# Optimization experiments

Measured on AMD Instinct MI355X. Metric: run time of the kernel, lower is better.

## Reference

```python
import jax, jax.numpy as jnp
import numpy as np

N_HEADS = 4


def grid_sample_bilinear(img, grid):
    # img: (B, C, H, W); grid: (B, *S, 2) with (x, y) in [-1, 1]; torch bilinear, align_corners=True
    B, C, H, W = img.shape
    sp = grid.shape[1:-1]
    g = grid.reshape(B, -1, 2)
    x = (g[..., 0] + 1.0) * 0.5 * (W - 1)
    y = (g[..., 1] + 1.0) * 0.5 * (H - 1)
    x0 = jnp.floor(x)
    y0 = jnp.floor(y)
    wx = x - x0
    wy = y - y0
    x0i = jnp.clip(x0, 0, W - 1).astype(jnp.int32)
    x1i = jnp.clip(x0 + 1, 0, W - 1).astype(jnp.int32)
    y0i = jnp.clip(y0, 0, H - 1).astype(jnp.int32)
    y1i = jnp.clip(y0 + 1, 0, H - 1).astype(jnp.int32)
    flat = img.reshape(B, C, H * W)
    take = jax.vmap(lambda f, i: f[:, i])  # (C, HW), (N,) -> (C, N)
    out = (take(flat, y0i * W + x0i) * ((1 - wx) * (1 - wy))[:, None, :]
           + take(flat, y0i * W + x1i) * (wx * (1 - wy))[:, None, :]
           + take(flat, y1i * W + x0i) * ((1 - wx) * wy)[:, None, :]
           + take(flat, y1i * W + x1i) * (wx * wy)[:, None, :])
    return out.reshape((B, C) + sp)


def dw_conv_k4s4(x, w, b):
    # depthwise conv, kernel=4, stride=4, pad=0 (kernel == stride): non-overlapping patches
    B, C, H, W = x.shape
    xr = x.reshape(B, C, H // 4, 4, W // 4, 4)
    return jnp.einsum('bchpwq,cpq->bchw', xr, w) + b[None, :, None, None]


def ln_channels(x, g, b, eps=1e-5):
    # LayerNormProxy: LayerNorm over channel dim of NCHW
    mu = jnp.mean(x, axis=1, keepdims=True)
    var = jnp.var(x, axis=1, keepdims=True)
    return (x - mu) * jax.lax.rsqrt(var + eps) * g[None, :, None, None] + b[None, :, None, None]


def ref_points(Hk, Wk):
    ry = jnp.linspace(0.5, Hk - 0.5, Hk) / (Hk - 1.0) * 2.0 - 1.0
    rx = jnp.linspace(0.5, Wk - 0.5, Wk) / (Wk - 1.0) * 2.0 - 1.0
    return jnp.stack(jnp.meshgrid(ry, rx, indexing='ij'), axis=-1)  # (Hk, Wk, 2) as (y, x)


def q_grid(H, W):
    ry = jnp.arange(H, dtype=jnp.float32) / (H - 1.0) * 2.0 - 1.0
    rx = jnp.arange(W, dtype=jnp.float32) / (W - 1.0) * 2.0 - 1.0
    return jnp.stack(jnp.meshgrid(ry, rx, indexing='ij'), axis=-1).reshape(H * W, 2)


def dat_block(x, p):
    # DAttentionBaseline: n_groups=1, stride=ksize=4, offset_range_factor=-1, use_pe (learned rpe table)
    dw_w, dw_b, ln_g, ln_b, pw_w, wq, bq, wk, bk, wv, bv, wo, bo, rpe = p
    B, C, H, W = x.shape
    hc = C // N_HEADS
    scale = hc ** -0.5
    q = jnp.einsum('oc,bchw->bohw', wq, x) + bq[None, :, None, None]
    t = jax.nn.gelu(ln_channels(dw_conv_k4s4(q, dw_w, dw_b), ln_g, ln_b), approximate=False)
    off = jnp.einsum('oc,bchw->bohw', pw_w, t)  # (B, 2, Hk, Wk), channels = (dy, dx)
    Hk, Wk = off.shape[2], off.shape[3]
    ns = Hk * Wk
    pos = jnp.clip(off.transpose(0, 2, 3, 1) + ref_points(Hk, Wk)[None], -1.0, 1.0)  # (B,Hk,Wk,2) (y,x)
    xs = grid_sample_bilinear(x, pos[..., ::-1]).reshape(B, C, ns)  # kv == q input here
    k = jnp.einsum('oc,bcn->bon', wk, xs) + bk[None, :, None]
    v = jnp.einsum('oc,bcn->bon', wv, xs) + bv[None, :, None]
    qh = q.reshape(B, N_HEADS, hc, H * W)
    attn = jnp.einsum('bhcm,bhcn->bhmn', qh, k.reshape(B, N_HEADS, hc, ns)) * scale
    disp = (q_grid(H, W)[None, :, None, :] - pos.reshape(B, 1, ns, 2)) * 0.5  # (B, HW, ns, 2) (y,x)
    rpe_b = jnp.broadcast_to(rpe[None], (B,) + rpe.shape)
    attn = attn + grid_sample_bilinear(rpe_b, disp[..., ::-1])  # (B, heads, HW, ns)
    attn = jax.nn.softmax(attn, axis=-1)
    out = jnp.einsum('bhmn,bhcn->bhcm', attn, v.reshape(B, N_HEADS, hc, ns)).reshape(B, C, H, W)
    return jnp.einsum('oc,bchw->bohw', wo, out) + bo[None, :, None, None]


def _block_params(key, c, H, W):
    ks = jax.random.split(key, 7)
    return dict(
        off_dw_w=0.05 * jax.random.normal(ks[0], (c, 4, 4), dtype=jnp.float32),
        off_dw_b=jnp.zeros((c,), jnp.float32),
        ln_g=jnp.ones((c,), jnp.float32),
        ln_b=jnp.zeros((c,), jnp.float32),
        off_pw_w=0.02 * jax.random.normal(ks[1], (2, c), dtype=jnp.float32),
        wq=0.02 * jax.random.normal(ks[2], (c, c), dtype=jnp.float32),
        bq=jnp.zeros((c,), jnp.float32),
        wk=0.02 * jax.random.normal(ks[3], (c, c), dtype=jnp.float32),
        bk=jnp.zeros((c,), jnp.float32),
        wv=0.02 * jax.random.normal(ks[4], (c, c), dtype=jnp.float32),
        bv=jnp.zeros((c,), jnp.float32),
        wo=0.02 * jax.random.normal(ks[5], (c, c), dtype=jnp.float32),
        bo=jnp.zeros((c,), jnp.float32),
        rpe=0.01 * jax.random.normal(ks[6], (N_HEADS, 2 * H - 1, 2 * W - 1), dtype=jnp.float32),
    )


def setup_inputs() -> dict:
    key = jax.random.key(0)
    k0, k1, k2 = jax.random.split(key, 3)
    B, C, H, W = 8, 512, 64, 64
    inp = {'x0': jax.random.normal(k0, (B, C, H, W), dtype=jnp.float32)}
    for pre, k in (('sc_', k1), ('tr_', k2)):
        for n, v in _block_params(k, C // 2, H, W).items():
            inp[pre + n] = v
    return inp


def reference(x0,
              sc_off_dw_w, sc_off_dw_b, sc_ln_g, sc_ln_b, sc_off_pw_w, sc_wq, sc_bq, sc_wk, sc_bk,
              sc_wv, sc_bv, sc_wo, sc_bo, sc_rpe,
              tr_off_dw_w, tr_off_dw_b, tr_ln_g, tr_ln_b, tr_off_pw_w, tr_wq, tr_bq, tr_wk, tr_bk,
              tr_wv, tr_bv, tr_wo, tr_bo, tr_rpe):
    B, C, H, W = x0.shape
    qc1 = C // 2
    q = x0[:, :qc1]
    sc_p = (sc_off_dw_w, sc_off_dw_b, sc_ln_g, sc_ln_b, sc_off_pw_w, sc_wq, sc_bq, sc_wk, sc_bk,
            sc_wv, sc_bv, sc_wo, sc_bo, sc_rpe)
    tr_p = (tr_off_dw_w, tr_off_dw_b, tr_ln_g, tr_ln_b, tr_off_pw_w, tr_wq, tr_bq, tr_wk, tr_bk,
            tr_wv, tr_bv, tr_wo, tr_bo, tr_rpe)
    s = dat_block(q, sc_p)
    t = dat_block(q, tr_p)
    z = jnp.zeros((B, C - qc1, H, W), x0.dtype)
    scale_full = jnp.concatenate([z, s], axis=1)
    trans_full = jnp.concatenate([z, t], axis=1)
    res = x0 * jnp.exp(scale_full) + trans_full
    jac = jnp.sum(scale_full, axis=(1, 2, 3))[None, :]  # (n_vars=1, B)
    return res, jac
```

## Files before the change

### kernel.cpp

```cpp
#include <hip/hip_runtime.h>
#include <math.h>

typedef __bf16 bf16;
typedef __attribute__((ext_vector_type(8))) __bf16 bf16x8;
typedef __attribute__((ext_vector_type(4))) __bf16 bf16x4;
typedef __attribute__((ext_vector_type(4))) float floatx4;

#define MFMA16(a, b, c) __builtin_amdgcn_mfma_f32_16x16x32_bf16((a), (b), (c), 0, 0, 0)

__device__ __forceinline__ float bflo(unsigned d) {
    unsigned u = d << 16; float f; __builtin_memcpy(&f, &u, 4); return f;
}
__device__ __forceinline__ float bfhi(unsigned d) {
    unsigned u = d & 0xffff0000u; float f; __builtin_memcpy(&f, &u, 4); return f;
}

__device__ __forceinline__ void breduce1(float &a, float* lds, int t) {
    #pragma unroll
    for (int off = 32; off; off >>= 1) a += __shfl_xor(a, off, 64);
    __syncthreads();
    if ((t & 63) == 0) lds[t >> 6] = a;
    __syncthreads();
    a = lds[0] + lds[1] + lds[2] + lds[3];
}

__global__ __launch_bounds__(256) void init_kernel(const float* __restrict__ x0,
                                                   float* __restrict__ out) {
    int fi = blockIdx.x * 256 + threadIdx.x;
    int b = fi >> 18;
    int r = fi & 262143;
    const float4* src = (const float4*)x0;
    float4* dst = (float4*)out;
    dst[(size_t)b * 524288 + r] = src[(size_t)b * 524288 + r];
}

__global__ __launch_bounds__(256) void wconv(
    const float* __restrict__ w0, const float* __restrict__ w1,
    const float* __restrict__ w2, const float* __restrict__ w3,
    const float* __restrict__ w4, const float* __restrict__ w5,
    const float* __restrict__ w6, const float* __restrict__ w7,
    bf16* __restrict__ dst) {
    const int wi = blockIdx.y;
    const float* src = wi == 0 ? w0 : wi == 1 ? w1 : wi == 2 ? w2 : wi == 3 ? w3
                     : wi == 4 ? w4 : wi == 5 ? w5 : wi == 6 ? w6 : w7;
    const int i = blockIdx.x * 1024 + threadIdx.x * 4;
    const float4 v = *(const float4*)(src + i);
    bf16x4 h, l;
    #pragma unroll
    for (int j = 0; j < 4; j++) {
        const float f = ((const float*)&v)[j];
        const bf16 hb = (bf16)f;
        h[j] = hb;
        l[j] = (bf16)(f - (float)hb);
    }
    *(bf16x4*)(dst + (size_t)wi * 65536 + i) = h;
    *(bf16x4*)(dst + (size_t)(8 + wi) * 65536 + i) = l;
}

template <int MODE>
__global__ __launch_bounds__(256) void gemm_mfma(
    const void* __restrict__ Aptr, int ldA, long long bsA,
    const bf16* __restrict__ Whi, const bf16* __restrict__ Wlo,
    const float* __restrict__ bias,
    bf16* __restrict__ outb,
    float* outf,
    const float* __restrict__ x0full,
    float* __restrict__ jpart)
{
    constexpr bool ASPLIT = (MODE <= 2);
    __shared__ __align__(16) bf16 As_hi[128 * 40];
    __shared__ __align__(16) bf16 As_lo[ASPLIT ? 128 * 40 : 1];
    __shared__ __align__(16) bf16 Bs_hi[128 * 40];
    __shared__ __align__(16) bf16 Bs_lo[128 * 40];
    __shared__ float red[4];
    const int t = threadIdx.x;
    const int b = blockIdx.z;
    const int n0 = blockIdx.x * 128;
    const int o0 = blockIdx.y * 128;
    const int w = t >> 6, l = t & 63;
    const int wr = w & 1, wc = w >> 1;
    const int lr = l & 15, lq = l >> 4;

    floatx4 acc[4][4] = {};

    for (int kb = 0; kb < 8; kb++) {
        if (ASPLIT) {
            const float* Af = (const float*)Aptr + (size_t)b * bsA;
            #pragma unroll
            for (int s = 0; s < 4; s++) {
                const int kk = s * 8 + (t >> 5);
                const int n = (t & 31) * 4;
                const float4 v = *(const float4*)(Af + (size_t)(kb * 32 + kk) * ldA + n0 + n);
                #pragma unroll
                for (int j = 0; j < 4; j++) {
                    const float f = ((const float*)&v)[j];
                    const bf16 hb = (bf16)f;
                    As_hi[(n + j) * 40 + kk] = hb;
                    As_lo[(n + j) * 40 + kk] = (bf16)(f - (float)hb);
                }
            }
        } else {
            const bf16* Ab = (const bf16*)Aptr + (size_t)b * bsA;
            #pragma unroll
            for (int s = 0; s < 2; s++) {
                const int idx = t + 256 * s;
                const int row = idx >> 2, seg = idx & 3;
                *(bf16x8*)(As_hi + row * 40 + seg * 8) =
                    *(const bf16x8*)(Ab + (size_t)(n0 + row) * 256 + kb * 32 + seg * 8);
            }
        }
        #pragma unroll
        for (int s = 0; s < 2; s++) {
            const int idx = t + 256 * s;
            const int row = idx >> 2, seg = idx & 3;
            *(bf16x8*)(Bs_hi + row * 40 + seg * 8) =
                *(const bf16x8*)(Whi + (size_t)(o0 + row) * 256 + kb * 32 + seg * 8);
            *(bf16x8*)(Bs_lo + row * 40 + seg * 8) =
                *(const bf16x8*)(Wlo + (size_t)(o0 + row) * 256 + kb * 32 + seg * 8);
        }
        __syncthreads();
        bf16x8 ah[4], al[4], bh[4], bl[4];
        #pragma unroll
        for (int f = 0; f < 4; f++) {
            ah[f] = *(const bf16x8*)(As_hi + (wr * 64 + f * 16 + lr) * 40 + lq * 8);
            if (ASPLIT)
                al[f] = *(const bf16x8*)(As_lo + (wr * 64 + f * 16 + lr) * 40 + lq * 8);
            bh[f] = *(const bf16x8*)(Bs_hi + (wc * 64 + f * 16 + lr) * 40 + lq * 8);
            bl[f] = *(const bf16x8*)(Bs_lo + (wc * 64 + f * 16 + lr) * 40 + lq * 8);
        }
        #pragma unroll
        for (int i = 0; i < 4; i++)
            #pragma unroll
            for (int j = 0; j < 4; j++) {
                acc[i][j] = MFMA16(ah[i], bh[j], acc[i][j]);
                acc[i][j] = MFMA16(ah[i], bl[j], acc[i][j]);
                if (ASPLIT) acc[i][j] = MFMA16(al[i], bh[j], acc[i][j]);
            }
        __syncthreads();
    }

    float ssum = 0.0f;
    #pragma unroll
    for (int i = 0; i < 4; i++) {
        #pragma unroll
        for (int j = 0; j < 4; j++) {
            const int o_g = o0 + wc * 64 + j * 16 + lr;
            const int n_b = n0 + wr * 64 + i * 16 + lq * 4;
            const float bia = bias[o_g];
            floatx4 val = acc[i][j];
            val[0] += bia; val[1] += bia; val[2] += bia; val[3] += bia;
            if (MODE == 0) {
                *(floatx4*)(outf + (size_t)b * 2097152 + (size_t)o_g * 4096 + n_b) = val;
                #pragma unroll
                for (int r = 0; r < 4; r++)
                    outb[((size_t)b * 4096 + n_b + r) * 256 + o_g] = (bf16)val[r];
            } else {
                const size_t addr = (size_t)b * 2097152 + (size_t)(256 + o_g) * 4096 + n_b;
                if (MODE == 3) {
                    *(floatx4*)(outf + addr) = val;
                } else {
                    const floatx4 s4 = *(const floatx4*)(outf + addr);
                    const floatx4 x4 = *(const floatx4*)(x0full + addr);
                    floatx4 res;
                    #pragma unroll
                    for (int r = 0; r < 4; r++) res[r] = x4[r] * expf(s4[r]) + val[r];
                    *(floatx4*)(outf + addr) = res;
                    ssum += s4[0] + s4[1] + s4[2] + s4[3];
                }
            }
        }
    }
    if (MODE == 4) {
        breduce1(ssum, red, t);
        if (t == 0) jpart[b * 64 + blockIdx.y * 32 + blockIdx.x] = ssum;
    }
}

__global__ __launch_bounds__(256) void gemm_kv(
    const bf16* __restrict__ xs_hi, const bf16* __restrict__ xs_lo,
    const bf16* __restrict__ wkh, const bf16* __restrict__ wkl,
    const bf16* __restrict__ wvh, const bf16* __restrict__ wvl,
    const float* __restrict__ bk, const float* __restrict__ bv,
    bf16* __restrict__ kT, bf16* __restrict__ vbuf)
{
    __shared__ __align__(16) bf16 As_hi[128 * 40];
    __shared__ __align__(16) bf16 As_lo[128 * 40];
    __shared__ __align__(16) bf16 Bs_hi[128 * 40];
    __shared__ __align__(16) bf16 Bs_lo[128 * 40];
    const int t = threadIdx.x;
    const int b = blockIdx.z;
    const int n0 = blockIdx.x * 128;
    const int kv = blockIdx.y >> 1;
    const int o0 = (blockIdx.y & 1) * 128;
    const bf16* Whi = kv ? wvh : wkh;
    const bf16* Wlo = kv ? wvl : wkl;
    const float* bias = kv ? bv : bk;
    const int w = t >> 6, l = t & 63;
    const int wr = w & 1, wc = w >> 1;
    const int lr = l & 15, lq = l >> 4;

    floatx4 acc[4][4] = {};

    for (int kb = 0; kb < 8; kb++) {
        #pragma unroll
        for (int s = 0; s < 2; s++) {
            const int idx = t + 256 * s;
            const int row = idx >> 2, seg = idx & 3;
            const size_t asrc = ((size_t)b * 256 + n0 + row) * 256 + kb * 32 + seg * 8;
            *(bf16x8*)(As_hi + row * 40 + seg * 8) = *(const bf16x8*)(xs_hi + asrc);
            *(bf16x8*)(As_lo + row * 40 + seg * 8) = *(const bf16x8*)(xs_lo + asrc);
            *(bf16x8*)(Bs_hi + row * 40 + seg * 8) =
                *(const bf16x8*)(Whi + (size_t)(o0 + row) * 256 + kb * 32 + seg * 8);
            *(bf16x8*)(Bs_lo + row * 40 + seg * 8) =
                *(const bf16x8*)(Wlo + (size_t)(o0 + row) * 256 + kb * 32 + seg * 8);
        }
        __syncthreads();
        bf16x8 ah[4], al[4], bh[4], bl[4];
        #pragma unroll
        for (int f = 0; f < 4; f++) {
            ah[f] = *(const bf16x8*)(As_hi + (wr * 64 + f * 16 + lr) * 40 + lq * 8);
            al[f] = *(const bf16x8*)(As_lo + (wr * 64 + f * 16 + lr) * 40 + lq * 8);
            bh[f] = *(const bf16x8*)(Bs_hi + (wc * 64 + f * 16 + lr) * 40 + lq * 8);
            bl[f] = *(const bf16x8*)(Bs_lo + (wc * 64 + f * 16 + lr) * 40 + lq * 8);
        }
        #pragma unroll
        for (int i = 0; i < 4; i++)
            #pragma unroll
            for (int j = 0; j < 4; j++) {
                acc[i][j] = MFMA16(ah[i], bh[j], acc[i][j]);
                acc[i][j] = MFMA16(ah[i], bl[j], acc[i][j]);
                acc[i][j] = MFMA16(al[i], bh[j], acc[i][j]);
            }
        __syncthreads();
    }

    #pragma unroll
    for (int i = 0; i < 4; i++) {
        #pragma unroll
        for (int j = 0; j < 4; j++) {
            const int o_g = o0 + wc * 64 + j * 16 + lr;
            const int n_b = n0 + wr * 64 + i * 16 + lq * 4;
            const float bia = bias[o_g];
            floatx4 val = acc[i][j];
            val[0] += bia; val[1] += bia; val[2] += bia; val[3] += bia;
            if (kv == 0) {
                #pragma unroll
                for (int r = 0; r < 4; r++)
                    kT[((size_t)b * 256 + n_b + r) * 256 + o_g] = (bf16)val[r];
            } else {
                bf16x4 pv;
                pv[0] = (bf16)val[0]; pv[1] = (bf16)val[1];
                pv[2] = (bf16)val[2]; pv[3] = (bf16)val[3];
                *(bf16x4*)(vbuf + ((size_t)b * 256 + o_g) * 256 + n_b) = pv;
            }
        }
    }
}

__global__ __launch_bounds__(64) void jac_reduce(const float* __restrict__ jpart,
                                                 float* __restrict__ out) {
    const int b = blockIdx.x, t = threadIdx.x;
    float v = jpart[b * 64 + t];
    #pragma unroll
    for (int off = 32; off; off >>= 1) v += __shfl_xor(v, off, 64);
    if (t == 0) out[16777216 + b] = v;
}

__global__ __launch_bounds__(256) void offset_kernel(
    const float* __restrict__ q,
    const float* __restrict__ dw_w, const float* __restrict__ dw_b,
    const float* __restrict__ ln_g, const float* __restrict__ ln_b,
    const float* __restrict__ pw_w,
    float* __restrict__ pos)
{
    __shared__ float red[8];
    const int wk = blockIdx.x, hk = blockIdx.y, b = blockIdx.z;
    const int c = threadIdx.x;
    const float* qp = q + (size_t)b * 2097152 + (size_t)c * 4096 + (hk * 4) * 64 + wk * 4;
    float accv = dw_b[c];
    #pragma unroll
    for (int p = 0; p < 4; p++) {
        const float4 r = *(const float4*)(qp + p * 64);
        const float4 w = *(const float4*)(dw_w + c * 16 + p * 4);
        accv += r.x * w.x + r.y * w.y + r.z * w.z + r.w * w.w;
    }
    float a = accv, sq = accv * accv;
    #pragma unroll
    for (int off = 32; off; off >>= 1) {
        a += __shfl_xor(a, off, 64);
        sq += __shfl_xor(sq, off, 64);
    }
    __syncthreads();
    if ((c & 63) == 0) { red[c >> 6] = a; red[4 + (c >> 6)] = sq; }
    __syncthreads();
    a = red[0] + red[1] + red[2] + red[3];
    sq = red[4] + red[5] + red[6] + red[7];
    const float mu = a * (1.0f / 256.0f);
    const float var = sq * (1.0f / 256.0f) - mu * mu;
    float nrm = (accv - mu) * rsqrtf(var + 1e-5f) * ln_g[c] + ln_b[c];
    const float act = 0.5f * nrm * (1.0f + erff(nrm * 0.70710678118654752f));
    float v0 = pw_w[c] * act;
    float v1 = pw_w[256 + c] * act;
    #pragma unroll
    for (int off = 32; off; off >>= 1) {
        v0 += __shfl_xor(v0, off, 64);
        v1 += __shfl_xor(v1, off, 64);
    }
    __syncthreads();
    if ((c & 63) == 0) { red[c >> 6] = v0; red[4 + (c >> 6)] = v1; }
    __syncthreads();
    if (c == 0) {
        v0 = red[0] + red[1] + red[2] + red[3];
        v1 = red[4] + red[5] + red[6] + red[7];
        const float refy = (0.5f + hk) * (2.0f / 15.0f) - 1.0f;
        const float refx = (0.5f + wk) * (2.0f / 15.0f) - 1.0f;
        const float py = fminf(fmaxf(v0 + refy, -1.0f), 1.0f);
        const float px = fminf(fmaxf(v1 + refx, -1.0f), 1.0f);
        const int n = hk * 16 + wk;
        pos[(b * 256 + n) * 2] = py;
        pos[(b * 256 + n) * 2 + 1] = px;
    }
}

__global__ __launch_bounds__(256) void sample_kernel(
    const float* __restrict__ x0,
    const float* __restrict__ pos,
    bf16* __restrict__ xs_hi,
    bf16* __restrict__ xs_lo)
{
    const int c = threadIdx.x, n = blockIdx.x, b = blockIdx.y;
    const float py = pos[(b * 256 + n) * 2];
    const float px = pos[(b * 256 + n) * 2 + 1];
    const float x = (px + 1.0f) * 31.5f;
    const float y = (py + 1.0f) * 31.5f;
    const float xf = floorf(x), yf = floorf(y);
    const float wx = x - xf, wy = y - yf;
    const int xi0 = min(max((int)xf, 0), 63);
    const int xi1 = min(xi0 + 1, 63);
    const int yi0 = min(max((int)yf, 0), 63);
    const int yi1 = min(yi0 + 1, 63);
    const float* base = x0 + (size_t)b * 2097152 + (size_t)c * 4096;
    const float v00 = base[yi0 * 64 + xi0], v01 = base[yi0 * 64 + xi1];
    const float v10 = base[yi1 * 64 + xi0], v11 = base[yi1 * 64 + xi1];
    const float f =
        v00 * (1 - wx) * (1 - wy) + v01 * wx * (1 - wy) +
        v10 * (1 - wx) * wy + v11 * wx * wy;
    const bf16 hb = (bf16)f;
    const size_t addr = ((size_t)b * 256 + n) * 256 + c;
    xs_hi[addr] = hb;
    xs_lo[addr] = (bf16)(f - (float)hb);
}

__global__ __launch_bounds__(256, 4) void attn_mfma(
    const bf16* qbfT,
    const bf16* __restrict__ kT,
    const bf16* __restrict__ vb,
    const float* __restrict__ pos,
    const float* __restrict__ rpe,
    bf16* obfT)
{
    __shared__ __align__(16) bf16 pl[16896];
    __shared__ float wxs[256];
    const int t = threadIdx.x;
    const int w = t >> 6, l = t & 63;
    const int lr = l & 15, lq = l >> 4;
    const int m_base = blockIdx.x * 64 + w * 16;
    const int my = blockIdx.x;
    const int h = blockIdx.y, b = blockIdx.z;

    const float2 pp = *(const float2*)(pos + (b * 256 + t) * 2);
    const float yy = (float)my + 63.0f - 31.5f * pp.x;
    const float xo = 63.0f - 31.5f * pp.y;
    const float yfl = floorf(yy);
    const float wy_r = yy - yfl;
    const int y0 = min((int)yfl, 126);
    const int o0_r = y0 * 127;
    const int o1_r = min(y0 + 1, 126) * 127;
    const int xb_r = (int)floorf(xo);
    wxs[t] = xo - (float)xb_r;

    const float* rp = rpe + h * 16129;

    const bf16* qrow = qbfT + ((size_t)b * 4096 + m_base + lr) * 256 + h * 64;
    const bf16x8 qf0 = *(const bf16x8*)(qrow + lq * 8);
    const bf16x8 qf1 = *(const bf16x8*)(qrow + 32 + lq * 8);

    #pragma unroll 8
    for (int i = 0; i < 64; i++) {
        const int xb = __shfl(xb_r, i);
        const float wy = __shfl(wy_r, i);
        const int o0 = __shfl(o0_r, i);
        const int o1 = __shfl(o1_r, i);
        const int xj = min(xb + l, 126);
        const float v0 = rp[o0 + xj];
        const float v1 = rp[o1 + xj];
        pl[(w * 64 + i) * 66 + l] = (bf16)fmaf(wy, v1 - v0, v0);
    }
    {
        const int xe = min(xb_r + 64, 126);
        const float e0 = rp[o0_r + xe];
        const float e1 = rp[o1_r + xe];
        pl[t * 66 + 64] = (bf16)fmaf(wy_r, e1 - e0, e0);
    }

    floatx4 lg[16];
    #pragma unroll
    for (int nf = 0; nf < 16; nf++) {
        const bf16* krow = kT + ((size_t)b * 256 + nf * 16 + lr) * 256 + h * 64;
        const bf16x8 k0 = *(const bf16x8*)(krow + lq * 8);
        const bf16x8 k1 = *(const bf16x8*)(krow + 32 + lq * 8);
        floatx4 a = {};
        a = MFMA16(qf0, k0, a);
        a = MFMA16(qf1, k1, a);
        lg[nf] = a;
    }

    bf16x8 vpre[2][4];
    #pragma unroll
    for (int kf = 0; kf < 2; kf++)
        #pragma unroll
        for (int j = 0; j < 4; j++)
            vpre[kf][j] = *(const bf16x8*)(
                vb + ((size_t)b * 256 + h * 64 + j * 16 + lr) * 256 + kf * 32 + lq * 8);

    __syncthreads();

    #pragma unroll
    for (int nf = 0; nf < 16; nf++) {
        const int n = nf * 16 + lr;
        const unsigned* rw = (const unsigned*)(pl + n * 66 + w * 16 + lq * 4);
        const unsigned d0 = rw[0], d1 = rw[1], d2 = rw[2];
        float rv[5];
        rv[0] = bflo(d0); rv[1] = bfhi(d0);
        rv[2] = bflo(d1); rv[3] = bfhi(d1);
        rv[4] = bflo(d2);
        const float wxv = wxs[n];
        #pragma unroll
        for (int r = 0; r < 4; r++)
            lg[nf][r] = lg[nf][r] * 0.125f + (rv[r] + wxv * (rv[r + 1] - rv[r]));
    }

    float mx[4], inv[4];
    #pragma unroll
    for (int r = 0; r < 4; r++) {
        float m = -1e30f;
        #pragma unroll
        for (int nf = 0; nf < 16; nf++) m = fmaxf(m, lg[nf][r]);
        #pragma unroll
        for (int off = 1; off < 16; off <<= 1) m = fmaxf(m, __shfl_xor(m, off, 64));
        mx[r] = m;
    }
    #pragma unroll
    for (int r = 0; r < 4; r++) {
        float s = 0.0f;
        #pragma unroll
        for (int nf = 0; nf < 16; nf++) {
            const float e = __expf(lg[nf][r] - mx[r]);
            lg[nf][r] = e;
            s += e;
        }
        #pragma unroll
        for (int off = 1; off < 16; off <<= 1) s += __shfl_xor(s, off, 64);
        inv[r] = 1.0f / s;
    }

    __syncthreads();

    bf16* plw = pl + w * 16 * 264;
    #pragma unroll
    for (int nf = 0; nf < 16; nf++)
        #pragma unroll
        for (int r = 0; r < 4; r++)
            plw[(lq * 4 + r) * 264 + nf * 16 + lr] = (bf16)(lg[nf][r] * inv[r]);

    floatx4 oc[4] = {};
    #pragma unroll
    for (int kf = 0; kf < 8; kf++) {
        const bf16x8 pa = *(const bf16x8*)(plw + lr * 264 + kf * 32 + lq * 8);
        #pragma unroll
        for (int j = 0; j < 4; j++) {
            const bf16x8 vf = (kf < 2) ? vpre[kf][j] : *(const bf16x8*)(
                vb + ((size_t)b * 256 + h * 64 + j * 16 + lr) * 256 + kf * 32 + lq * 8);
            oc[j] = MFMA16(pa, vf, oc[j]);
        }
    }

    bf16* ot = plw;
    #pragma unroll
    for (int j = 0; j < 4; j++)
        #pragma unroll
        for (int r = 0; r < 4; r++)
            ot[(lq * 4 + r) * 72 + j * 16 + lr] = (bf16)oc[j][r];
    const int mrow = l >> 2, seg = l & 3;
    const bf16x8 ov0 = *(const bf16x8*)(ot + mrow * 72 + seg * 8);
    const bf16x8 ov1 = *(const bf16x8*)(ot + mrow * 72 + (4 + seg) * 8);
    bf16* orow = obfT + ((size_t)b * 4096 + m_base + mrow) * 256 + h * 64;
    *(bf16x8*)(orow + seg * 8) = ov0;
    *(bf16x8*)(orow + (4 + seg) * 8) = ov1;
}

extern "C" void kernel_launch(void* const* d_in, const int* in_sizes, int n_in,
                              void* d_out, int out_size, void* d_ws, size_t ws_size,
                              hipStream_t stream) {
    const float* x0 = (const float*)d_in[0];
    float* out = (float*)d_out;
    float* ws = (float*)d_ws;
    bf16* qbfT  = (bf16*)ws;
    bf16* xs_hi = (bf16*)(ws + 4194304);
    bf16* xs_lo = xs_hi + 524288;
    bf16* kTb   = (bf16*)(ws + 4718592);
    bf16* vbb   = (bf16*)(ws + 4980736);
    bf16* wbf   = (bf16*)(ws + 5242880);
    float* pos  = ws + 5767168;
    float* jpart= ws + 5771264;

    wconv<<<dim3(64, 8), 256, 0, stream>>>(
        (const float*)d_in[6], (const float*)d_in[8], (const float*)d_in[10],
        (const float*)d_in[12], (const float*)d_in[20], (const float*)d_in[22],
        (const float*)d_in[24], (const float*)d_in[26], wbf);

    for (int pass = 0; pass < 2; pass++) {
        const int pb = 1 + 14 * pass;
        const float* dw_w = (const float*)d_in[pb + 0];
        const float* dw_b = (const float*)d_in[pb + 1];
        const float* ln_g = (const float*)d_in[pb + 2];
        const float* ln_b = (const float*)d_in[pb + 3];
        const float* pw_w = (const float*)d_in[pb + 4];
        const float* bq   = (const float*)d_in[pb + 6];
        const float* bk   = (const float*)d_in[pb + 8];
        const float* bv   = (const float*)d_in[pb + 10];
        const float* bo   = (const float*)d_in[pb + 12];
        const float* rpe  = (const float*)d_in[pb + 13];
        const bf16* wq_h = wbf + (size_t)(pass * 4 + 0) * 65536;
        const bf16* wk_h = wbf + (size_t)(pass * 4 + 1) * 65536;
        const bf16* wv_h = wbf + (size_t)(pass * 4 + 2) * 65536;
        const bf16* wo_h = wbf + (size_t)(pass * 4 + 3) * 65536;
        const bf16* wq_l = wq_h + 8 * 65536;
        const bf16* wk_l = wk_h + 8 * 65536;
        const bf16* wv_l = wv_h + 8 * 65536;
        const bf16* wo_l = wo_h + 8 * 65536;

        gemm_mfma<0><<<dim3(32, 2, 8), 256, 0, stream>>>(
            x0, 4096, 2097152LL, wq_h, wq_l, bq, qbfT, out, nullptr, nullptr);
        offset_kernel<<<dim3(16, 16, 8), 256, 0, stream>>>(
            out, dw_w, dw_b, ln_g, ln_b, pw_w, pos);
        sample_kernel<<<dim3(256, 8), 256, 0, stream>>>(x0, pos, xs_hi, xs_lo);
        gemm_kv<<<dim3(2, 4, 8), 256, 0, stream>>>(
            xs_hi, xs_lo, wk_h, wk_l, wv_h, wv_l, bk, bv, kTb, vbb);
        attn_mfma<<<dim3(64, 4, 8), 256, 0, stream>>>(
            qbfT, kTb, vbb, pos, rpe, qbfT);
        if (pass == 0)
            gemm_mfma<3><<<dim3(32, 2, 8), 256, 0, stream>>>(
                qbfT, 256, 1048576LL, wo_h, wo_l, bo, nullptr, out, nullptr, nullptr);
        else
            gemm_mfma<4><<<dim3(32, 2, 8), 256, 0, stream>>>(
                qbfT, 256, 1048576LL, wo_h, wo_l, bo, nullptr, out, x0, jpart);
    }
    init_kernel<<<8192, 256, 0, stream>>>(x0, out);
    jac_reduce<<<8, 64, 0, stream>>>(jpart, out);
}
```

Before: 615.1 us.

## Split attention over keys into two chunks with online softmax

Restructures the attention kernel to process the 256 keys in two chunks of 128, using a running max and sum (online softmax) and rescaling the output accumulators between chunks. This halves the live logits registers and the per-wave probability buffer in LDS, and it drops the preloaded V fragments. The aim is lower register and LDS pressure and so higher occupancy. The cost is extra exp and rescale work, and the V loads are no longer prefetched ahead of the softmax.

After: 624.7 us. No clear change (+1.6%).

```diff
diff --git a/kernel.cpp b/kernel.cpp
--- a/kernel.cpp
+++ b/kernel.cpp
@@ -402,95 +402,95 @@
         const float e1 = rp[o1_r + xe];
         pl[t * 66 + 64] = (bf16)fmaf(wy_r, e1 - e0, e0);
     }
-
-    floatx4 lg[16];
-    #pragma unroll
-    for (int nf = 0; nf < 16; nf++) {
-        const bf16* krow = kT + ((size_t)b * 256 + nf * 16 + lr) * 256 + h * 64;
-        const bf16x8 k0 = *(const bf16x8*)(krow + lq * 8);
-        const bf16x8 k1 = *(const bf16x8*)(krow + 32 + lq * 8);
-        floatx4 a = {};
-        a = MFMA16(qf0, k0, a);
-        a = MFMA16(qf1, k1, a);
-        lg[nf] = a;
-    }
-
-    bf16x8 vpre[2][4];
-    #pragma unroll
-    for (int kf = 0; kf < 2; kf++)
-        #pragma unroll
-        for (int j = 0; j < 4; j++)
-            vpre[kf][j] = *(const bf16x8*)(
-                vb + ((size_t)b * 256 + h * 64 + j * 16 + lr) * 256 + kf * 32 + lq * 8);
-
-    __syncthreads();
-
-    #pragma unroll
-    for (int nf = 0; nf < 16; nf++) {
-        const int n = nf * 16 + lr;
-        const unsigned* rw = (const unsigned*)(pl + n * 66 + w * 16 + lq * 4);
-        const unsigned d0 = rw[0], d1 = rw[1], d2 = rw[2];
-        float rv[5];
-        rv[0] = bflo(d0); rv[1] = bfhi(d0);
-        rv[2] = bflo(d1); rv[3] = bfhi(d1);
-        rv[4] = bflo(d2);
-        const float wxv = wxs[n];
+    __syncthreads();
+
+    float mrun[4] = {-1e30f, -1e30f, -1e30f, -1e30f};
+    float srun[4] = {0.0f, 0.0f, 0.0f, 0.0f};
+    floatx4 oc[4] = {};
+    bf16* plw = pl + w * 2112;
+
+    #pragma unroll
+    for (int c = 0; c < 2; c++) {
+        floatx4 lg[8];
+        #pragma unroll
+        for (int nf = 0; nf < 8; nf++) {
+            const bf16* krow = kT + ((size_t)b * 256 + c * 128 + nf * 16 + lr) * 256 + h * 64;
+            const bf16x8 k0 = *(const bf16x8*)(krow + lq * 8);
+            const bf16x8 k1 = *(const bf16x8*)(krow + 32 + lq * 8);
+            floatx4 a = {};
+            a = MFMA16(qf0, k0, a);
+            a = MFMA16(qf1, k1, a);
+            lg[nf] = a;
+        }
+
+        #pragma unroll
+        for (int nf = 0; nf < 8; nf++) {
+            const int n = c * 128 + nf * 16 + lr;
+            const unsigned* rw = (const unsigned*)(pl + n * 66 + w * 16 + lq * 4);
+            const unsigned d0 = rw[0], d1 = rw[1], d2 = rw[2];
+            float rv[5];
+            rv[0] = bflo(d0); rv[1] = bfhi(d0);
+            rv[2] = bflo(d1); rv[3] = bfhi(d1);
+            rv[4] = bflo(d2);
+            const float wxv = wxs[n];
+            #pragma unroll
+            for (int r = 0; r < 4; r++)
+                lg[nf][r] = lg[nf][r] * 0.125f + (rv[r] + wxv * (rv[r + 1] - rv[r]));
+        }
+
+        #pragma unroll
+        for (int r = 0; r < 4; r++) {
+            float m = lg[0][r];
+            #pragma unroll
+            for (int nf = 1; nf < 8; nf++) m = fmaxf(m, lg[nf][r]);
+            #pragma unroll
+            for (int off = 1; off < 16; off <<= 1) m = fmaxf(m, __shfl_xor(m, off, 64));
+            const float mn = fmaxf(mrun[r], m);
+            const float sc = __expf(mrun[r] - mn);
+            mrun[r] = mn;
+            float s = 0.0f;
+            #pragma unroll
+            for (int nf = 0; nf < 8; nf++) {
+                const float e = __expf(lg[nf][r] - mn);
+                lg[nf][r] = e;
+                s += e;
+            }
+            #pragma unroll
+            for (int off = 1; off < 16; off <<= 1) s += __shfl_xor(s, off, 64);
+            srun[r] = srun[r] * sc + s;
+            oc[0][r] *= sc; oc[1][r] *= sc; oc[2][r] *= sc; oc[3][r] *= sc;
+        }
+
+        if (c == 0) __syncthreads();
+
+        #pragma unroll
+        for (int nf = 0; nf < 8; nf++)
+            #pragma unroll
+            for (int r = 0; r < 4; r++)
+                plw[(lq * 4 + r) * 132 + nf * 16 + lr] = (bf16)lg[nf][r];
+
+        #pragma unroll
+        for (int kf = 0; kf < 4; kf++) {
+            const bf16x8 pa = *(const bf16x8*)(plw + lr * 132 + kf * 32 + lq * 8);
+            #pragma unroll
+            for (int j = 0; j < 4; j++) {
+                const bf16x8 vf = *(const bf16x8*)(
+                    vb + ((size_t)b * 256 + h * 64 + j * 16 + lr) * 256 + c * 128 + kf * 32 + lq * 8);
+                oc[j] = MFMA16(pa, vf, oc[j]);
+            }
+        }
+    }
+
+    float inv[4];
+    #pragma unroll
+    for (int r = 0; r < 4; r++) inv[r] = 1.0f / srun[r];
+
+    bf16* ot = plw;
+    #pragma unroll
+    for (int j = 0; j < 4; j++)
         #pragma unroll
         for (int r = 0; r < 4; r++)
-            lg[nf][r] = lg[nf][r] * 0.125f + (rv[r] + wxv * (rv[r + 1] - rv[r]));
-    }
-
-    float mx[4], inv[4];
-    #pragma unroll
-    for (int r = 0; r < 4; r++) {
-        float m = -1e30f;
-        #pragma unroll
-        for (int nf = 0; nf < 16; nf++) m = fmaxf(m, lg[nf][r]);
-        #pragma unroll
-        for (int off = 1; off < 16; off <<= 1) m = fmaxf(m, __shfl_xor(m, off, 64));
-        mx[r] = m;
-    }
-    #pragma unroll
-    for (int r = 0; r < 4; r++) {
-        float s = 0.0f;
-        #pragma unroll
-        for (int nf = 0; nf < 16; nf++) {
-            const float e = __expf(lg[nf][r] - mx[r]);
-            lg[nf][r] = e;
-            s += e;
-        }
-        #pragma unroll
-        for (int off = 1; off < 16; off <<= 1) s += __shfl_xor(s, off, 64);
-        inv[r] = 1.0f / s;
-    }
-
-    __syncthreads();
-
-    bf16* plw = pl + w * 16 * 264;
-    #pragma unroll
-    for (int nf = 0; nf < 16; nf++)
-        #pragma unroll
-        for (int r = 0; r < 4; r++)
-            plw[(lq * 4 + r) * 264 + nf * 16 + lr] = (bf16)(lg[nf][r] * inv[r]);
-
-    floatx4 oc[4] = {};
-    #pragma unroll
-    for (int kf = 0; kf < 8; kf++) {
-        const bf16x8 pa = *(const bf16x8*)(plw + lr * 264 + kf * 32 + lq * 8);
-        #pragma unroll
-        for (int j = 0; j < 4; j++) {
-            const bf16x8 vf = (kf < 2) ? vpre[kf][j] : *(const bf16x8*)(
-                vb + ((size_t)b * 256 + h * 64 + j * 16 + lr) * 256 + kf * 32 + lq * 8);
-            oc[j] = MFMA16(pa, vf, oc[j]);
-        }
-    }
-
-    bf16* ot = plw;
-    #pragma unroll
-    for (int j = 0; j < 4; j++)
-        #pragma unroll
-        for (int r = 0; r < 4; r++)
-            ot[(lq * 4 + r) * 72 + j * 16 + lr] = (bf16)oc[j][r];
+            ot[(lq * 4 + r) * 72 + j * 16 + lr] = (bf16)(oc[j][r] * inv[r]);
     const int mrow = l >> 2, seg = l & 3;
     const bf16x8 ov0 = *(const bf16x8*)(ot + mrow * 72 + seg * 8);
     const bf16x8 ov1 = *(const bf16x8*)(ot + mrow * 72 + (4 + seg) * 8);
```
